# Kernel optimization log

Hardware: AMD Instinct MI355X
Metric: run time of the kernel (lower is better)

The kernel has to match this reference:

```python
import jax, jax.numpy as jnp
import numpy as np

D_MODEL = 1024
N_HEADS = 16
HEAD_DIM = D_MODEL // N_HEADS
MAX_DEPTH = 4
EPS = 1e-06


def setup_inputs() -> dict:
    key = jax.random.key(0)
    ks = jax.random.split(key, 9)
    B, T, C = 8, 1024, D_MODEL
    s = 0.02
    return {
        "x": jax.random.normal(ks[0], (B, T, C), dtype=jnp.float32),
        "depths": jax.random.randint(ks[1], (B, T), 0, MAX_DEPTH, dtype=jnp.int64),
        "probs": jax.random.uniform(ks[2], (B, T, MAX_DEPTH), dtype=jnp.float32),
        "norm1_w": jnp.ones((C,), dtype=jnp.float32),
        "qkv_w": jax.random.normal(ks[3], (3 * C, C), dtype=jnp.float32) * s,
        "out_w": jax.random.normal(ks[4], (C, C), dtype=jnp.float32) * s,
        "norm2_w": jnp.ones((C,), dtype=jnp.float32),
        "fc1_w": jax.random.normal(ks[5], (4 * C, C), dtype=jnp.float32) * s,
        "fc2_w": jax.random.normal(ks[6], (C, 4 * C), dtype=jnp.float32) * s,
    }


def _rmsnorm(x, w):
    rms = jnp.sqrt(jnp.mean(x * x, axis=-1, keepdims=True) + EPS)
    return x / rms * w


def _attn(x, qkv_w, out_w):
    B, T, C = x.shape
    qkv = x @ qkv_w.T  # (B,T,3C)
    q, k, v = jnp.split(qkv, 3, axis=-1)
    def rs(t):
        return t.reshape(B, T, N_HEADS, HEAD_DIM).transpose(0, 2, 1, 3)  # (B,H,T,hd)
    q, k, v = rs(q), rs(k), rs(v)
    scores = jnp.einsum("bhqd,bhkd->bhqk", q, k) / jnp.sqrt(jnp.float32(HEAD_DIM))
    attn = jax.nn.softmax(scores, axis=-1)
    o = jnp.einsum("bhqk,bhkd->bhqd", attn, v)
    o = o.transpose(0, 2, 1, 3).reshape(B, T, C)
    return o @ out_w.T


def _apply_once(x, norm1_w, qkv_w, out_w, norm2_w, fc1_w, fc2_w):
    x = x + _attn(_rmsnorm(x, norm1_w), qkv_w, out_w)
    h = _rmsnorm(x, norm2_w)
    x = x + jax.nn.gelu(h @ fc1_w.T, approximate=False) @ fc2_w.T
    return x


def reference(x, depths, probs, norm1_w, qkv_w, out_w, norm2_w, fc1_w, fc2_w):
    # soft mode: weighted combination of outputs at depths 1..MAX_DEPTH
    cur = x
    outputs = []
    for _ in range(MAX_DEPTH):  # fixed small loop over depth levels
        cur = _apply_once(cur, norm1_w, qkv_w, out_w, norm2_w, fc1_w, fc2_w)
        outputs.append(cur)
    stacked = jnp.stack(outputs, axis=0)  # (D,B,T,C)
    return jnp.einsum("dbtc,btd->btc", stacked, probs)
```

## Files before the change

kernel.cpp:

```cpp
#include <hip/hip_runtime.h>
#include <cstdint>
#include <cstddef>

typedef __attribute__((ext_vector_type(8))) short bf16x8;
typedef __attribute__((ext_vector_type(4))) float f32x4;

#define DEV __device__ __forceinline__

DEV unsigned short f2bf(float f) {
  union { float f; unsigned u; } v; v.f = f;
  unsigned r = (v.u + 0x7FFFu + ((v.u >> 16) & 1u)) >> 16;
  return (unsigned short)r;
}

DEV unsigned short f2bf_rtz(float f) {
  union { float f; unsigned u; } v; v.f = f;
  return (unsigned short)(v.u >> 16);
}

DEV float bf2f(unsigned short h) {
  union { unsigned u; float f; } v; v.u = ((unsigned)h) << 16;
  return v.f;
}

DEV float gelu_fast(float x) {
  float x2 = x * x;
  float arg = x * fmaf(x2, 0.10294936f, 2.3021174f);
  float u = exp2f(arg);
  return x - x / (1.0f + u);
}

DEV void gload16(const void* g, void* l) {
  __builtin_amdgcn_global_load_lds(
      (__attribute__((address_space(1))) void*)const_cast<void*>(g),
      (__attribute__((address_space(3))) void*)l,
      16, 0, 0);
}


__global__ __launch_bounds__(256) void f2bf_kernel(const float* __restrict__ in,
                                                   unsigned short* __restrict__ out, int n4) {
  int i = blockIdx.x * 256 + threadIdx.x;
  if (i < n4) {
    float4 v = ((const float4*)in)[i];
    ushort4 o;
    o.x = f2bf(v.x); o.y = f2bf(v.y); o.z = f2bf(v.z); o.w = f2bf(v.w);
    ((ushort4*)out)[i] = o;
  }
}

__global__ __launch_bounds__(256) void rmsnorm_kernel(const unsigned short* __restrict__ x,
                                                      const float* __restrict__ w,
                                                      unsigned short* __restrict__ o) {
  const int row = blockIdx.x;
  const int tid = threadIdx.x;
  ushort4 u = ((const ushort4*)x)[(size_t)row * 256 + tid];
  float4 v;
  v.x = bf2f(u.x); v.y = bf2f(u.y); v.z = bf2f(u.z); v.w = bf2f(u.w);
  float s = v.x * v.x + v.y * v.y + v.z * v.z + v.w * v.w;
#pragma unroll
  for (int m = 32; m > 0; m >>= 1) s += __shfl_xor(s, m);
  __shared__ float red[4];
  if ((tid & 63) == 0) red[tid >> 6] = s;
  __syncthreads();
  float tot = red[0] + red[1] + red[2] + red[3];
  float inv = rsqrtf(tot * (1.0f / 1024.0f) + 1e-6f);
  float4 wv = ((const float4*)w)[tid];
  ushort4 ov;
  ov.x = f2bf(v.x * inv * wv.x);
  ov.y = f2bf(v.y * inv * wv.y);
  ov.z = f2bf(v.z * inv * wv.z);
  ov.w = f2bf(v.w * inv * wv.w);
  ((ushort4*)o)[(size_t)row * 256 + tid] = ov;
}

template <int EPI>
__global__ __launch_bounds__(256) void gemm_bf16(const unsigned short* __restrict__ A,
                                                 const unsigned short* __restrict__ W,
                                                 unsigned short* __restrict__ Of16,
                                                 const unsigned short* __restrict__ Res16,
                                                 float* __restrict__ OutAcc,
                                                 const float* __restrict__ probs,
                                                 int dIdx, int init,
                                                 int M, int N, int K) {
  __shared__ alignas(16) unsigned short As[128 * 64];
  __shared__ alignas(16) unsigned short Bs[128 * 64];
  const int tid = threadIdx.x;
  const int lane = tid & 63;
  const int wave = tid >> 6;
  const int wr = wave >> 1, wc = wave & 1;

  int bid = blockIdx.y * gridDim.x + blockIdx.x;
  const int nwg = gridDim.x * gridDim.y;
  bid = (bid & 7) * (nwg >> 3) + (bid >> 3);
  const int span = gridDim.x << 3;
  const int sg = bid / span;
  const int rem = bid % span;
  const int bx = rem >> 3;
  const int by = (sg << 3) + (rem & 7);

  const int brow = by * 128;
  const int bcol = bx * 128;

  f32x4 acc[4][4] = {};

  const int sr = tid >> 3;
  const int sc = ((tid & 7) ^ ((tid >> 3) & 7)) << 3;
  const int ro = lane & 15;
  const int rg = lane >> 4;
  const int rsw = (ro & 7) << 3;

  const unsigned short* aPtr = A + (size_t)(brow + sr) * K + sc;
  const unsigned short* wPtr = W + (size_t)(bcol + sr) * K + sc;
  const size_t rowStride32 = (size_t)32 * K;

  for (int kt = 0; kt < K; kt += 64) {
#pragma unroll
    for (int i = 0; i < 4; i++) {
      gload16(aPtr + i * rowStride32, &As[i * 2048 + wave * 512]);
      gload16(wPtr + i * rowStride32, &Bs[i * 2048 + wave * 512]);
    }
    aPtr += 64;
    wPtr += 64;
    __syncthreads();
#pragma unroll
    for (int kk = 0; kk < 2; kk++) {
      const int ko = kk * 32 + rg * 8;
      bf16x8 av[4], bv[4];
#pragma unroll
      for (int m2 = 0; m2 < 4; m2++)
        av[m2] = *(const bf16x8*)&As[(wr * 64 + m2 * 16 + ro) * 64 + (ko ^ rsw)];
#pragma unroll
      for (int n2 = 0; n2 < 4; n2++)
        bv[n2] = *(const bf16x8*)&Bs[(wc * 64 + n2 * 16 + ro) * 64 + (ko ^ rsw)];
#pragma unroll
      for (int m2 = 0; m2 < 4; m2++)
#pragma unroll
        for (int n2 = 0; n2 < 4; n2++)
          acc[m2][n2] = __builtin_amdgcn_mfma_f32_16x16x32_bf16(av[m2], bv[n2], acc[m2][n2], 0, 0, 0);
    }
    __syncthreads();
  }

#pragma unroll
  for (int m2 = 0; m2 < 4; m2++) {
#pragma unroll
    for (int i = 0; i < 4; i++) {
      const int row = brow + wr * 64 + m2 * 16 + rg * 4 + i;
#pragma unroll
      for (int n2 = 0; n2 < 4; n2++) {
        const int col = bcol + wc * 64 + n2 * 16 + ro;
        const size_t idx = (size_t)row * N + col;
        float v = acc[m2][n2][i];
        float nv = bf2f(Res16[idx]) + v;
        Of16[idx] = f2bf(nv);
        if (EPI == 3) {
          float p = probs[(size_t)row * 4 + dIdx];
          float o = init ? 0.f : OutAcc[idx];
          OutAcc[idx] = o + p * nv;
        }
      }
    }
  }
}

template <int EPI>
__global__ __launch_bounds__(256, 2) void gemm_m256(const unsigned short* __restrict__ A,
                                                    const unsigned short* __restrict__ W,
                                                    unsigned short* __restrict__ Ob,
                                                    int M, int N, int K) {
  __shared__ alignas(16) unsigned short As[256 * 64];
  __shared__ alignas(16) unsigned short Bs[128 * 64];
  const int tid = threadIdx.x;
  const int lane = tid & 63;
  const int wave = tid >> 6;
  const int wr = wave >> 1, wc = wave & 1;

  int bid = blockIdx.y * gridDim.x + blockIdx.x;
  const int nwg = gridDim.x * gridDim.y;
  bid = (bid & 7) * (nwg >> 3) + (bid >> 3);
  const int span = gridDim.x << 3;
  const int sg = bid / span;
  const int rem = bid % span;
  const int bx = rem >> 3;
  const int by = (sg << 3) + (rem & 7);

  const int brow = by * 256;
  const int bcol = bx * 128;

  f32x4 acc[8][4] = {};

  const int sr = tid >> 3;
  const int sc = ((tid & 7) ^ ((tid >> 3) & 7)) << 3;
  const int ro = lane & 15;
  const int rg = lane >> 4;
  const int rsw = (ro & 7) << 3;

  const unsigned short* aPtr = A + (size_t)(brow + sr) * K + sc;
  const unsigned short* wPtr = W + (size_t)(bcol + sr) * K + sc;
  const size_t rowStride32 = (size_t)32 * K;

  for (int kt = 0; kt < K; kt += 64) {
#pragma unroll
    for (int i = 0; i < 8; i++)
      gload16(aPtr + i * rowStride32, &As[i * 2048 + wave * 512]);
#pragma unroll
    for (int i = 0; i < 4; i++)
      gload16(wPtr + i * rowStride32, &Bs[i * 2048 + wave * 512]);
    aPtr += 64;
    wPtr += 64;
    __syncthreads();
#pragma unroll
    for (int kk = 0; kk < 2; kk++) {
      const int ko = kk * 32 + rg * 8;
      bf16x8 av[8], bv[4];
#pragma unroll
      for (int m2 = 0; m2 < 8; m2++)
        av[m2] = *(const bf16x8*)&As[(wr * 128 + m2 * 16 + ro) * 64 + (ko ^ rsw)];
#pragma unroll
      for (int n2 = 0; n2 < 4; n2++)
        bv[n2] = *(const bf16x8*)&Bs[(wc * 64 + n2 * 16 + ro) * 64 + (ko ^ rsw)];
#pragma unroll
      for (int m2 = 0; m2 < 8; m2++)
#pragma unroll
        for (int n2 = 0; n2 < 4; n2++)
          acc[m2][n2] = __builtin_amdgcn_mfma_f32_16x16x32_bf16(av[m2], bv[n2], acc[m2][n2], 0, 0, 0);
    }
    __syncthreads();
  }

#pragma unroll
  for (int m2 = 0; m2 < 8; m2++) {
#pragma unroll
    for (int i = 0; i < 4; i++) {
      const int row = brow + wr * 128 + m2 * 16 + rg * 4 + i;
#pragma unroll
      for (int n2 = 0; n2 < 4; n2++) {
        const int col = bcol + wc * 64 + n2 * 16 + ro;
        const size_t idx = (size_t)row * N + col;
        float v = acc[m2][n2][i];
        if (EPI == 0) {
          float s2 = (col < 1024) ? 0.18033688f : 1.0f;
          Ob[idx] = f2bf(v * s2);
        } else {
          Ob[idx] = f2bf(gelu_fast(v));
        }
      }
    }
  }
}

__global__ __launch_bounds__(512, 4) void attn_kernel(const unsigned short* __restrict__ qkv,
                                                      unsigned short* __restrict__ ob) {
  __shared__ alignas(16) unsigned short kt[64][72];
  __shared__ alignas(16) unsigned short vt[64][72];
  __shared__ alignas(16) unsigned short pt[8][16][72];
  const int tid = threadIdx.x, lane = tid & 63, wave = tid >> 6;

  const int nwg = gridDim.x * gridDim.y;
  int bid = blockIdx.y * gridDim.x + blockIdx.x;
  bid = (bid & 7) * (nwg >> 3) + (bid >> 3);
  const int qt = bid % gridDim.x;
  const int bh = bid / gridDim.x;
  const int b = bh >> 4, h = bh & 15;

  const size_t base = (size_t)b * 1024 * 3072 + (size_t)h * 64;
  const unsigned short* qp = qkv + base;
  const int q0 = qt * 128 + wave * 16;
  const int ro = lane & 15, rg = lane >> 4;

  bf16x8 aq[2];
  aq[0] = *(const bf16x8*)&qp[(size_t)(q0 + ro) * 3072 + rg * 8];
  aq[1] = *(const bf16x8*)&qp[(size_t)(q0 + ro) * 3072 + 32 + rg * 8];

  const int sr0 = tid >> 3, sci = tid & 7, scl = sci << 3;
  const unsigned short* kRow = qkv + base + 1024 + (size_t)sr0 * 3072 + scl;
  const unsigned short* vRow = qkv + base + 2048 + (size_t)sr0 * 3072 + scl;

  f32x4 oacc[4] = {};
  float mrow[4] = {-1e30f, -1e30f, -1e30f, -1e30f};
  float lrow[4] = {0.f, 0.f, 0.f, 0.f};

  for (int t0 = 0; t0 < 1024; t0 += 64) {
    {
      uint4 k0 = *(const uint4*)kRow;
      uint4 v0 = *(const uint4*)vRow;
      *(uint4*)&kt[sr0][scl] = k0;
      const unsigned short* e0 = (const unsigned short*)&v0;
#pragma unroll
      for (int j = 0; j < 8; j++) {
        const int jj = (j + sci) & 7;
        vt[scl + jj][sr0] = e0[jj];
      }
      kRow += 64 * 3072;
      vRow += 64 * 3072;
    }
    __syncthreads();

    f32x4 sf[4] = {};
#pragma unroll
    for (int kk = 0; kk < 2; kk++) {
      const int ko = kk * 32 + rg * 8;
#pragma unroll
      for (int n2 = 0; n2 < 4; n2++) {
        bf16x8 bk = *(const bf16x8*)&kt[n2 * 16 + ro][ko];
        sf[n2] = __builtin_amdgcn_mfma_f32_16x16x32_bf16(aq[kk], bk, sf[n2], 0, 0, 0);
      }
    }

    float lmax[4];
#pragma unroll
    for (int i = 0; i < 4; i++)
      lmax[i] = fmaxf(fmaxf(sf[0][i], sf[1][i]), fmaxf(sf[2][i], sf[3][i]));
    bool need = (lmax[0] > mrow[0] + 8.f) | (lmax[1] > mrow[1] + 8.f) |
                (lmax[2] > mrow[2] + 8.f) | (lmax[3] > mrow[3] + 8.f);
    if (__any(need)) {
#pragma unroll
      for (int msk = 1; msk < 16; msk <<= 1)
#pragma unroll
        for (int i = 0; i < 4; i++) lmax[i] = fmaxf(lmax[i], __shfl_xor(lmax[i], msk));
#pragma unroll
      for (int i = 0; i < 4; i++) {
        float mn = fmaxf(mrow[i], lmax[i]);
        float alpha = exp2f(mrow[i] - mn);
        mrow[i] = mn;
        lrow[i] *= alpha;
#pragma unroll
        for (int n2 = 0; n2 < 4; n2++) oacc[n2][i] *= alpha;
      }
    }
#pragma unroll
    for (int n2 = 0; n2 < 4; n2++)
#pragma unroll
      for (int i = 0; i < 4; i++) {
        sf[n2][i] = exp2f(sf[n2][i] - mrow[i]);
        lrow[i] += sf[n2][i];
      }

#pragma unroll
    for (int n2 = 0; n2 < 4; n2++)
#pragma unroll
      for (int i = 0; i < 4; i++)
        pt[wave][rg * 4 + i][n2 * 16 + ro] = f2bf_rtz(sf[n2][i]);
    asm volatile("" ::: "memory");

#pragma unroll
    for (int kk = 0; kk < 2; kk++) {
      const int ko = kk * 32 + rg * 8;
      bf16x8 ap = *(const bf16x8*)&pt[wave][ro][ko];
#pragma unroll
      for (int n2 = 0; n2 < 4; n2++) {
        bf16x8 bv2 = *(const bf16x8*)&vt[n2 * 16 + ro][ko];
        oacc[n2] = __builtin_amdgcn_mfma_f32_16x16x32_bf16(ap, bv2, oacc[n2], 0, 0, 0);
      }
    }
    __syncthreads();
  }

#pragma unroll
  for (int msk = 1; msk < 16; msk <<= 1)
#pragma unroll
    for (int i = 0; i < 4; i++) lrow[i] += __shfl_xor(lrow[i], msk);

#pragma unroll
  for (int n2 = 0; n2 < 4; n2++)
#pragma unroll
    for (int i = 0; i < 4; i++) {
      const int qrow = q0 + rg * 4 + i;
      float v = oacc[n2][i] / lrow[i];
      ob[((size_t)b * 1024 + qrow) * 1024 + h * 64 + n2 * 16 + ro] = f2bf(v);
    }
}


extern "C" void kernel_launch(void* const* d_in, const int* in_sizes, int n_in,
                              void* d_out, int out_size, void* d_ws, size_t ws_size,
                              hipStream_t stream) {
  const float* x = (const float*)d_in[0];
  const float* probs = (const float*)d_in[2];
  const float* n1w = (const float*)d_in[3];
  const float* qkvw = (const float*)d_in[4];
  const float* outw = (const float*)d_in[5];
  const float* n2w = (const float*)d_in[6];
  const float* fc1w = (const float*)d_in[7];
  const float* fc2w = (const float*)d_in[8];
  float* out = (float*)d_out;

  const int B = 8, T = 1024, C = 1024;
  const int M = B * T;

  char* ws = (char*)d_ws;
  size_t off = 0;
  auto alloc = [&](size_t bytes) {
    void* p = ws + off;
    off += (bytes + 255) & ~(size_t)255;
    return p;
  };
  unsigned short* wqkv = (unsigned short*)alloc((size_t)3072 * 1024 * 2);
  unsigned short* wout = (unsigned short*)alloc((size_t)1024 * 1024 * 2);
  unsigned short* wfc1 = (unsigned short*)alloc((size_t)4096 * 1024 * 2);
  unsigned short* wfc2 = (unsigned short*)alloc((size_t)1024 * 4096 * 2);
  unsigned short* xb = (unsigned short*)alloc((size_t)M * C * 2);
  unsigned short* xn = (unsigned short*)alloc((size_t)M * C * 2);
  char* big = (char*)alloc((size_t)M * 4096 * 2);
  unsigned short* qkvb = (unsigned short*)big;
  unsigned short* obuf = (unsigned short*)(big + (size_t)M * 3072 * 2);
  unsigned short* gbuf = (unsigned short*)big;

  f2bf_kernel<<<(3072 * 1024 / 4 + 255) / 256, 256, 0, stream>>>(qkvw, wqkv, 3072 * 1024 / 4);
  f2bf_kernel<<<(1024 * 1024 / 4 + 255) / 256, 256, 0, stream>>>(outw, wout, 1024 * 1024 / 4);
  f2bf_kernel<<<(4096 * 1024 / 4 + 255) / 256, 256, 0, stream>>>(fc1w, wfc1, 4096 * 1024 / 4);
  f2bf_kernel<<<(4096 * 1024 / 4 + 255) / 256, 256, 0, stream>>>(fc2w, wfc2, 4096 * 1024 / 4);
  f2bf_kernel<<<(M * C / 4 + 255) / 256, 256, 0, stream>>>(x, xb, M * C / 4);

  for (int d = 0; d < 4; d++) {
    rmsnorm_kernel<<<M, 256, 0, stream>>>(xb, n1w, xn);
    gemm_m256<0><<<dim3(3072 / 128, M / 256), 256, 0, stream>>>(xn, wqkv, qkvb, M, 3072, 1024);
    attn_kernel<<<dim3(T / 128, B * 16), 512, 0, stream>>>(qkvb, obuf);
    gemm_bf16<2><<<dim3(1024 / 128, M / 128), 256, 0, stream>>>(
        obuf, wout, xb, xb, nullptr, nullptr, 0, 0, M, 1024, 1024);
    rmsnorm_kernel<<<M, 256, 0, stream>>>(xb, n2w, xn);
    gemm_m256<1><<<dim3(4096 / 128, M / 256), 256, 0, stream>>>(xn, wfc1, gbuf, M, 4096, 1024);
    gemm_bf16<3><<<dim3(1024 / 128, M / 128), 256, 0, stream>>>(
        gbuf, wfc2, xb, xb, out, probs, d, d == 0 ? 1 : 0, M, 1024, 4096);
  }
}
```

Measured before the change: 1.497 ms.

## Process 32 query rows per wave in attention to reuse K/V tiles

Each wave now handles two 16-row query sub-tiles (32 rows), so a workgroup covers 256 queries instead of 128 and the grid's query dimension is halved. Every K/V tile staged into shared memory, and the V fragments loaded from it, now serve twice as many query rows, which cuts global K/V traffic and LDS reads per unit of work. The cost is more registers per thread (doubled accumulators and softmax state), a larger P buffer in shared memory, and half as many workgroups, which may lower occupancy and latency hiding.

```diff
diff --git a/kernel.cpp b/kernel.cpp
--- a/kernel.cpp
+++ b/kernel.cpp
@@ -254,7 +254,7 @@
                                                       unsigned short* __restrict__ ob) {
   __shared__ alignas(16) unsigned short kt[64][72];
   __shared__ alignas(16) unsigned short vt[64][72];
-  __shared__ alignas(16) unsigned short pt[8][16][72];
+  __shared__ alignas(16) unsigned short pt[8][32][72];
   const int tid = threadIdx.x, lane = tid & 63, wave = tid >> 6;
 
   const int nwg = gridDim.x * gridDim.y;
@@ -266,20 +266,26 @@
 
   const size_t base = (size_t)b * 1024 * 3072 + (size_t)h * 64;
   const unsigned short* qp = qkv + base;
-  const int q0 = qt * 128 + wave * 16;
+  const int q0 = qt * 256 + wave * 32;
   const int ro = lane & 15, rg = lane >> 4;
 
-  bf16x8 aq[2];
-  aq[0] = *(const bf16x8*)&qp[(size_t)(q0 + ro) * 3072 + rg * 8];
-  aq[1] = *(const bf16x8*)&qp[(size_t)(q0 + ro) * 3072 + 32 + rg * 8];
+  bf16x8 aq[2][2];
+#pragma unroll
+  for (int m = 0; m < 2; m++) {
+    aq[m][0] = *(const bf16x8*)&qp[(size_t)(q0 + m * 16 + ro) * 3072 + rg * 8];
+    aq[m][1] = *(const bf16x8*)&qp[(size_t)(q0 + m * 16 + ro) * 3072 + 32 + rg * 8];
+  }
 
   const int sr0 = tid >> 3, sci = tid & 7, scl = sci << 3;
   const unsigned short* kRow = qkv + base + 1024 + (size_t)sr0 * 3072 + scl;
   const unsigned short* vRow = qkv + base + 2048 + (size_t)sr0 * 3072 + scl;
 
-  f32x4 oacc[4] = {};
-  float mrow[4] = {-1e30f, -1e30f, -1e30f, -1e30f};
-  float lrow[4] = {0.f, 0.f, 0.f, 0.f};
+  f32x4 oacc[2][4] = {};
+  float mrow[2][4], lrow[2][4];
+#pragma unroll
+  for (int m = 0; m < 2; m++)
+#pragma unroll
+    for (int i = 0; i < 4; i++) { mrow[m][i] = -1e30f; lrow[m][i] = 0.f; }
 
   for (int t0 = 0; t0 < 1024; t0 += 64) {
     {
@@ -297,79 +303,90 @@
     }
     __syncthreads();
 
-    f32x4 sf[4] = {};
+#pragma unroll
+    for (int m = 0; m < 2; m++) {
+      f32x4 sf[4] = {};
+#pragma unroll
+      for (int kk = 0; kk < 2; kk++) {
+        const int ko = kk * 32 + rg * 8;
+#pragma unroll
+        for (int n2 = 0; n2 < 4; n2++) {
+          bf16x8 bk = *(const bf16x8*)&kt[n2 * 16 + ro][ko];
+          sf[n2] = __builtin_amdgcn_mfma_f32_16x16x32_bf16(aq[m][kk], bk, sf[n2], 0, 0, 0);
+        }
+      }
+
+      float lmax[4];
+#pragma unroll
+      for (int i = 0; i < 4; i++)
+        lmax[i] = fmaxf(fmaxf(sf[0][i], sf[1][i]), fmaxf(sf[2][i], sf[3][i]));
+      bool need = (lmax[0] > mrow[m][0] + 8.f) | (lmax[1] > mrow[m][1] + 8.f) |
+                  (lmax[2] > mrow[m][2] + 8.f) | (lmax[3] > mrow[m][3] + 8.f);
+      if (__any(need)) {
+#pragma unroll
+        for (int msk = 1; msk < 16; msk <<= 1)
+#pragma unroll
+          for (int i = 0; i < 4; i++) lmax[i] = fmaxf(lmax[i], __shfl_xor(lmax[i], msk));
+#pragma unroll
+        for (int i = 0; i < 4; i++) {
+          float mn = fmaxf(mrow[m][i], lmax[i]);
+          float alpha = exp2f(mrow[m][i] - mn);
+          mrow[m][i] = mn;
+          lrow[m][i] *= alpha;
+#pragma unroll
+          for (int n2 = 0; n2 < 4; n2++) oacc[m][n2][i] *= alpha;
+        }
+      }
+#pragma unroll
+      for (int n2 = 0; n2 < 4; n2++)
+#pragma unroll
+        for (int i = 0; i < 4; i++) {
+          sf[n2][i] = exp2f(sf[n2][i] - mrow[m][i]);
+          lrow[m][i] += sf[n2][i];
+        }
+
+#pragma unroll
+      for (int n2 = 0; n2 < 4; n2++)
+#pragma unroll
+        for (int i = 0; i < 4; i++)
+          pt[wave][m * 16 + rg * 4 + i][n2 * 16 + ro] = f2bf_rtz(sf[n2][i]);
+    }
+    asm volatile("" ::: "memory");
+
 #pragma unroll
     for (int kk = 0; kk < 2; kk++) {
       const int ko = kk * 32 + rg * 8;
-#pragma unroll
-      for (int n2 = 0; n2 < 4; n2++) {
-        bf16x8 bk = *(const bf16x8*)&kt[n2 * 16 + ro][ko];
-        sf[n2] = __builtin_amdgcn_mfma_f32_16x16x32_bf16(aq[kk], bk, sf[n2], 0, 0, 0);
-      }
-    }
-
-    float lmax[4];
-#pragma unroll
-    for (int i = 0; i < 4; i++)
-      lmax[i] = fmaxf(fmaxf(sf[0][i], sf[1][i]), fmaxf(sf[2][i], sf[3][i]));
-    bool need = (lmax[0] > mrow[0] + 8.f) | (lmax[1] > mrow[1] + 8.f) |
-                (lmax[2] > mrow[2] + 8.f) | (lmax[3] > mrow[3] + 8.f);
-    if (__any(need)) {
-#pragma unroll
-      for (int msk = 1; msk < 16; msk <<= 1)
-#pragma unroll
-        for (int i = 0; i < 4; i++) lmax[i] = fmaxf(lmax[i], __shfl_xor(lmax[i], msk));
+      bf16x8 bv2[4];
+#pragma unroll
+      for (int n2 = 0; n2 < 4; n2++) bv2[n2] = *(const bf16x8*)&vt[n2 * 16 + ro][ko];
+#pragma unroll
+      for (int m = 0; m < 2; m++) {
+        bf16x8 ap = *(const bf16x8*)&pt[wave][m * 16 + ro][ko];
+#pragma unroll
+        for (int n2 = 0; n2 < 4; n2++)
+          oacc[m][n2] = __builtin_amdgcn_mfma_f32_16x16x32_bf16(ap, bv2[n2], oacc[m][n2], 0, 0, 0);
+      }
+    }
+    __syncthreads();
+  }
+
+#pragma unroll
+  for (int msk = 1; msk < 16; msk <<= 1)
+#pragma unroll
+    for (int m = 0; m < 2; m++)
+#pragma unroll
+      for (int i = 0; i < 4; i++) lrow[m][i] += __shfl_xor(lrow[m][i], msk);
+
+#pragma unroll
+  for (int m = 0; m < 2; m++)
+#pragma unroll
+    for (int n2 = 0; n2 < 4; n2++)
 #pragma unroll
       for (int i = 0; i < 4; i++) {
-        float mn = fmaxf(mrow[i], lmax[i]);
-        float alpha = exp2f(mrow[i] - mn);
-        mrow[i] = mn;
-        lrow[i] *= alpha;
-#pragma unroll
-        for (int n2 = 0; n2 < 4; n2++) oacc[n2][i] *= alpha;
-      }
-    }
-#pragma unroll
-    for (int n2 = 0; n2 < 4; n2++)
-#pragma unroll
-      for (int i = 0; i < 4; i++) {
-        sf[n2][i] = exp2f(sf[n2][i] - mrow[i]);
-        lrow[i] += sf[n2][i];
-      }
-
-#pragma unroll
-    for (int n2 = 0; n2 < 4; n2++)
-#pragma unroll
-      for (int i = 0; i < 4; i++)
-        pt[wave][rg * 4 + i][n2 * 16 + ro] = f2bf_rtz(sf[n2][i]);
-    asm volatile("" ::: "memory");
-
-#pragma unroll
-    for (int kk = 0; kk < 2; kk++) {
-      const int ko = kk * 32 + rg * 8;
-      bf16x8 ap = *(const bf16x8*)&pt[wave][ro][ko];
-#pragma unroll
-      for (int n2 = 0; n2 < 4; n2++) {
-        bf16x8 bv2 = *(const bf16x8*)&vt[n2 * 16 + ro][ko];
-        oacc[n2] = __builtin_amdgcn_mfma_f32_16x16x32_bf16(ap, bv2, oacc[n2], 0, 0, 0);
-      }
-    }
-    __syncthreads();
-  }
-
-#pragma unroll
-  for (int msk = 1; msk < 16; msk <<= 1)
-#pragma unroll
-    for (int i = 0; i < 4; i++) lrow[i] += __shfl_xor(lrow[i], msk);
-
-#pragma unroll
-  for (int n2 = 0; n2 < 4; n2++)
-#pragma unroll
-    for (int i = 0; i < 4; i++) {
-      const int qrow = q0 + rg * 4 + i;
-      float v = oacc[n2][i] / lrow[i];
-      ob[((size_t)b * 1024 + qrow) * 1024 + h * 64 + n2 * 16 + ro] = f2bf(v);
-    }
+        const int qrow = q0 + m * 16 + rg * 4 + i;
+        float v = oacc[m][n2][i] / lrow[m][i];
+        ob[((size_t)b * 1024 + qrow) * 1024 + h * 64 + n2 * 16 + ro] = f2bf(v);
+      }
 }
 
 
@@ -416,7 +433,7 @@
   for (int d = 0; d < 4; d++) {
     rmsnorm_kernel<<<M, 256, 0, stream>>>(xb, n1w, xn);
     gemm_m256<0><<<dim3(3072 / 128, M / 256), 256, 0, stream>>>(xn, wqkv, qkvb, M, 3072, 1024);
-    attn_kernel<<<dim3(T / 128, B * 16), 512, 0, stream>>>(qkvb, obuf);
+    attn_kernel<<<dim3(T / 256, B * 16), 512, 0, stream>>>(qkvb, obuf);
     gemm_bf16<2><<<dim3(1024 / 128, M / 128), 256, 0, stream>>>(
         obuf, wout, xb, xb, nullptr, nullptr, 0, 0, M, 1024, 1024);
     rmsnorm_kernel<<<M, 256, 0, stream>>>(xb, n2w, xn);
```

Measured after the change: 1.547 ms. 1.03x slower.
